# Optimization experiments

Measured on AMD Instinct MI355X. Metric: run time of the kernel, lower is better.

The kernel has to match this reference:

```python
import jax, jax.numpy as jnp
import numpy as np

D = 1024        # d_model
H = 16          # n_heads
DF = 4096       # d_ff
MAXL = 1024     # max_len
MAXSTEPS = 24   # max_steps


def setup_inputs() -> dict:
    key = jax.random.key(0)
    ks = jax.random.split(key, 10)
    B, S = 4, 1024
    s = 0.02
    f32 = jnp.float32
    return {
        "x": jax.random.normal(ks[0], (B, S, D), f32),
        "original_input": jax.random.normal(ks[1], (B, S, D), f32),
        "think_step": 5,
        "step_embed": jax.random.normal(ks[2], (MAXSTEPS, D), f32) * s,
        "Wqkv": jax.random.normal(ks[3], (D, 3 * D), f32) * s,
        "bqkv": jnp.zeros((3 * D,), f32),
        "Wout": jax.random.normal(ks[4], (D, D), f32) * s,
        "bout": jnp.zeros((D,), f32),
        "Wg": jax.random.normal(ks[5], (2 * D, D), f32) * s,
        "bg": jnp.zeros((D,), f32),
        "rel_pos_bias": jax.random.normal(ks[6], (2 * MAXL - 1,), f32) * s,
        "W1": jax.random.normal(ks[7], (D, DF), f32) * s,
        "b1": jnp.zeros((DF,), f32),
        "W2": jax.random.normal(ks[8], (DF, D), f32) * s,
        "b2": jnp.zeros((D,), f32),
        "ln1_g": jnp.ones((D,), f32),
        "ln1_b": jnp.zeros((D,), f32),
        "ln2_g": jnp.ones((D,), f32),
        "ln2_b": jnp.zeros((D,), f32),
    }


def _layer_norm(x, g, b, eps=1e-5):
    m = jnp.mean(x, axis=-1, keepdims=True)
    v = jnp.mean((x - m) ** 2, axis=-1, keepdims=True)
    return (x - m) * jax.lax.rsqrt(v + eps) * g + b


def reference(x, original_input, think_step, step_embed, Wqkv, bqkv, Wout, bout,
              Wg, bg, rel_pos_bias, W1, b1, W2, b2, ln1_g, ln1_b, ln2_g, ln2_b):
    B, S, _ = x.shape
    hd = D // H
    # gated residual input injection
    gate = jax.nn.sigmoid(jnp.concatenate([x, original_input], axis=-1) @ Wg + bg)
    x = x * (1.0 - gate) + original_input * gate
    # think-step embedding (clamped)
    step = min(int(think_step), MAXSTEPS - 1)
    x = x + step_embed[step][None, None, :]
    # qkv projection -> (3, B, H, S, hd)
    qkv = (x @ Wqkv + bqkv).reshape(B, S, 3, H, hd).transpose(2, 0, 3, 1, 4)
    q, k, v = qkv[0], qkv[1], qkv[2]
    scores = jnp.einsum('bhqd,bhkd->bhqk', q, k) * (hd ** -0.5)
    # relative position bias: dist clamped to [0, 2*MAXL-2]
    pos = jnp.arange(S)
    rel = jnp.clip(pos[:, None] - pos[None, :] + (MAXL - 1), 0, 2 * MAXL - 2)
    scores = scores + rel_pos_bias[rel][None, None]  # (B,H,S,S)
    probs = jax.nn.softmax(scores, axis=-1)
    attn = jnp.einsum('bhqk,bhkd->bhqd', probs, v)
    attn = attn.transpose(0, 2, 1, 3).reshape(B, S, D)
    attn = attn @ Wout + bout
    x = _layer_norm(x + attn, ln1_g, ln1_b)
    h = jax.nn.gelu(x @ W1 + b1, approximate=False) @ W2 + b2
    return _layer_norm(x + h, ln2_g, ln2_b)
```

## Files before the change

### kernel.cpp

```cpp
#include <hip/hip_runtime.h>
#include <hip/hip_bf16.h>
#include <math.h>

#define D_MODEL 1024
#define NH      16
#define HD      64
#define DFF     4096
#define SEQ     1024
#define BATCH   4
#define TOK     (BATCH*SEQ)
#define MAXSTEPS 24

typedef __hip_bfloat16 bf16;
typedef __attribute__((ext_vector_type(8))) short short8;
typedef __attribute__((ext_vector_type(4))) float floatx4;

__device__ __forceinline__ float b2f(bf16 v){ return __bfloat162float(v); }
__device__ __forceinline__ bf16  f2b(float v){ return __float2bfloat16(v); }

__device__ __forceinline__ void gload_lds16(const bf16* g, bf16* l){
    __builtin_amdgcn_global_load_lds((const __attribute__((address_space(1))) void*)g,
                                     (__attribute__((address_space(3))) void*)l, 16, 0, 0);
}

template<int TN, int EPI, bool SPLITK>
__global__ __launch_bounds__(256)
void mfma_gemm(const bf16* __restrict__ A, const bf16* __restrict__ Bt,
               const float* __restrict__ bias, void* __restrict__ outv,
               void* __restrict__ outv2,
               int M, int N, int K, int lda, int ldb,
               const float* __restrict__ xg, const float* __restrict__ og,
               const float* __restrict__ seg, const int* __restrict__ stepp)
{
    constexpr int NT  = TN / 32;
    constexpr int NBP = TN / 64;
    constexpr int R   = (TN == 64) ? 4 : 3;
    __shared__ bf16 As[R][128 * 32];
    __shared__ bf16 Bs[R][TN * 32];
    const int tid  = threadIdx.x;
    const int lane = tid & 63;
    const int w    = tid >> 6;
    const int wm   = w & 1, wn = w >> 1;
    const int fr   = lane & 15;
    const int q    = lane >> 4;

    if (SPLITK) {
        int z = blockIdx.z;
        A  += (size_t)z * K;
        Bt += (size_t)z * K;
    }

    const int tn_g = gridDim.x;
    const int nwg  = tn_g * gridDim.y;
    const int bid  = blockIdx.y * tn_g + blockIdx.x;
    const int o    = (bid & 7) * (nwg >> 3) + (bid >> 3);
    const int bandw = 8 * tn_g;
    const int band  = o / bandw;
    const int rr    = o - band * bandw;
    const int row0 = (band * 8 + (rr & 7)) * 128;
    const int col0 = (rr >> 3) * TN;

    const bf16* gA[2]; int sA_[2];
    #pragma unroll
    for (int p = 0; p < 2; ++p) {
        int s  = p * 256 + tid;
        int m  = s >> 2;
        int qg = (s & 3) ^ ((m >> 1) & 3);
        gA[p]  = A + (size_t)(row0 + m) * lda + qg * 8;
        sA_[p] = s * 8;
    }
    const bf16* gB[NBP]; int sB_[NBP];
    #pragma unroll
    for (int p = 0; p < NBP; ++p) {
        int s  = p * 256 + tid;
        int m  = s >> 2;
        int qg = (s & 3) ^ ((m >> 1) & 3);
        gB[p]  = Bt + (size_t)(col0 + m) * ldb + qg * 8;
        sB_[p] = s * 8;
    }

    int aoff[4], boff[NT];
    #pragma unroll
    for (int t = 0; t < 4; ++t) {
        int ml  = wm * 64 + t * 16 + fr;
        aoff[t] = (ml * 4 + (q ^ ((ml >> 1) & 3))) * 8;
    }
    #pragma unroll
    for (int t = 0; t < NT; ++t) {
        int nl  = wn * (TN / 2) + t * 16 + fr;
        boff[t] = (nl * 4 + (q ^ ((nl >> 1) & 3))) * 8;
    }

    #pragma unroll
    for (int pt = 0; pt < R - 1; ++pt) {
        #pragma unroll
        for (int p = 0; p < 2; ++p)   gload_lds16(gA[p] + pt * 32, &As[pt][sA_[p]]);
        #pragma unroll
        for (int p = 0; p < NBP; ++p) gload_lds16(gB[p] + pt * 32, &Bs[pt][sB_[p]]);
    }

    floatx4 acc[4][NT] = {};
    const int nk = K >> 5;
    int cur = 0;
    int kst = (R - 1) * 32;

    for (int t = 0; t < nk; ++t) {
        if constexpr (TN == 64) asm volatile("s_waitcnt vmcnt(6)" ::: "memory");
        else                    asm volatile("s_waitcnt vmcnt(4)" ::: "memory");
        __builtin_amdgcn_s_barrier();
        asm volatile("" ::: "memory");

        if (kst < K) {
            int sb = (cur == 0) ? (R - 1) : (cur - 1);
            #pragma unroll
            for (int p = 0; p < 2; ++p)   gload_lds16(gA[p] + kst, &As[sb][sA_[p]]);
            #pragma unroll
            for (int p = 0; p < NBP; ++p) gload_lds16(gB[p] + kst, &Bs[sb][sB_[p]]);
            kst += 32;
        }

        short8 af[4], bfg[NT];
        #pragma unroll
        for (int i = 0; i < 4; ++i)  af[i]  = *(const short8*)(&As[cur][aoff[i]]);
        #pragma unroll
        for (int j = 0; j < NT; ++j) bfg[j] = *(const short8*)(&Bs[cur][boff[j]]);
        #pragma unroll
        for (int i = 0; i < 4; ++i)
            #pragma unroll
            for (int j = 0; j < NT; ++j)
                acc[i][j] = __builtin_amdgcn_mfma_f32_16x16x32_bf16(af[i], bfg[j], acc[i][j], 0, 0, 0);

        cur = (cur == R - 1) ? 0 : (cur + 1);
    }

    void* outp = outv;
    float bscale = 1.0f;
    if (SPLITK && blockIdx.z != 0) { outp = outv2; bscale = 0.0f; }

    int st = 0;
    if (EPI == 3) {
        st = stepp[0];
        st = st < 0 ? 0 : (st > MAXSTEPS - 1 ? MAXSTEPS - 1 : st);
    }

    float bv[NT], sv[NT];
    #pragma unroll
    for (int nt = 0; nt < NT; ++nt) {
        int col = col0 + wn * (TN / 2) + nt * 16 + fr;
        bv[nt] = bias[col] * bscale;
        if (EPI == 3) sv[nt] = seg[st * D_MODEL + col];
    }
    #pragma unroll
    for (int mt = 0; mt < 4; ++mt) {
        #pragma unroll
        for (int nt = 0; nt < NT; ++nt) {
            int col = col0 + wn * (TN / 2) + nt * 16 + fr;
            #pragma unroll
            for (int r = 0; r < 4; ++r) {
                int row = row0 + wm * 64 + mt * 16 + q * 4 + r;
                float v = acc[mt][nt][r] + bv[nt];
                if (EPI == 0) {
                    ((float*)outp)[(size_t)row * N + col] = v;
                } else if (EPI == 1) {
                    ((bf16*)outp)[(size_t)row * N + col] = f2b(v);
                } else if (EPI == 2) {
                    float g = 0.5f * v * (1.0f + erff(v * 0.70710678118654752f));
                    ((bf16*)outp)[(size_t)row * N + col] = f2b(g);
                } else {
                    float g = 1.0f / (1.0f + __expf(-v));
                    size_t idx = (size_t)row * N + col;
                    float mix = xg[idx] * (1.0f - g) + og[idx] * g + sv[nt];
                    ((bf16*)outp)[idx] = f2b(mix);
                }
            }
        }
    }
}

#define NTRANS_BLOCKS 14336
__global__ __launch_bounds__(256)
void transpose_all_kernel(const float* __restrict__ Wg,   bf16* __restrict__ WgT,
                          const float* __restrict__ Wqkv, bf16* __restrict__ WqkvT,
                          const float* __restrict__ Wout, bf16* __restrict__ WoutT,
                          const float* __restrict__ W1,   bf16* __restrict__ W1T,
                          const float* __restrict__ W2,   bf16* __restrict__ W2T)
{
    __shared__ float t[32][33];
    const int bid = blockIdx.x;
    if (bid >= NTRANS_BLOCKS) return;
    const float* W; bf16* WT; int K, N, base;
    if      (bid <  2048) { W = Wg;   WT = WgT;   K = 2048; N = 1024; base = 0; }
    else if (bid <  5120) { W = Wqkv; WT = WqkvT; K = 1024; N = 3072; base = 2048; }
    else if (bid <  6144) { W = Wout; WT = WoutT; K = 1024; N = 1024; base = 5120; }
    else if (bid < 10240) { W = W1;   WT = W1T;   K = 1024; N = 4096; base = 6144; }
    else                  { W = W2;   WT = W2T;   K = 4096; N = 1024; base = 10240; }
    const int lb  = bid - base;
    const int ntx = N >> 5;
    const int n0 = (lb % ntx) * 32, k0 = (lb / ntx) * 32;
    const int tx = threadIdx.x & 31, ty = threadIdx.x >> 5;
    #pragma unroll
    for (int i = 0; i < 4; ++i)
        t[ty + i * 8][tx] = W[(size_t)(k0 + ty + i * 8) * N + n0 + tx];
    __syncthreads();
    #pragma unroll
    for (int i = 0; i < 4; ++i)
        WT[(size_t)(n0 + ty + i * 8) * K + k0 + tx] = f2b(t[tx][ty + i * 8]);
}

__global__ __launch_bounds__(256)
void vtrans_kernel(const bf16* __restrict__ qkv, bf16* __restrict__ Vt)
{
    __shared__ float t[32][33];
    const int blk = blockIdx.x;
    const int dt = blk & 1;
    const int st = (blk >> 1) & 31;
    const int h  = (blk >> 6) & 15;
    const int b  = blk >> 10;
    const int tx = threadIdx.x & 31, ty = threadIdx.x >> 5;
    #pragma unroll
    for (int i = 0; i < 4; ++i)
        t[ty + i * 8][tx] = b2f(qkv[(size_t)(b * SEQ + st * 32 + ty + i * 8) * 3072
                                    + 2048 + h * 64 + dt * 32 + tx]);
    __syncthreads();
    #pragma unroll
    for (int i = 0; i < 4; ++i)
        Vt[(size_t)((b * NH + h) * 64 + dt * 32 + ty + i * 8) * SEQ + st * 32 + tx]
            = f2b(t[tx][ty + i * 8]);
}

__global__ __launch_bounds__(256)
void xcat_kernel(const float* __restrict__ x, const float* __restrict__ orig,
                 bf16* __restrict__ xcat)
{
    int i = blockIdx.x * 256 + threadIdx.x;
    float4 xv = ((const float4*)x)[i];
    float4 ov = ((const float4*)orig)[i];
    int t = i >> 8, c4 = (i & 255) * 4;
    bf16* px = xcat + (size_t)t * 2048 + c4;
    px[0] = f2b(xv.x); px[1] = f2b(xv.y); px[2] = f2b(xv.z); px[3] = f2b(xv.w);
    bf16* po = px + 1024;
    po[0] = f2b(ov.x); po[1] = f2b(ov.y); po[2] = f2b(ov.z); po[3] = f2b(ov.w);
}

__global__ __launch_bounds__(256)
void fattn_kernel(const bf16* __restrict__ qkv, const bf16* __restrict__ Vt,
                  const float* __restrict__ relb, bf16* __restrict__ out)
{
    __shared__ bf16 KPs[128 * 64];
    __shared__ bf16 Vs [64 * 128];
    __shared__ float relb_s[1088];

    const int tid  = threadIdx.x;
    const int lane = tid & 63;
    const int w    = tid >> 6;
    const int fr   = lane & 15;
    const int quad = lane >> 4;

    const int qt = blockIdx.x & 15;
    const int h  = (blockIdx.x >> 4) & 15;
    const int b  = blockIdx.x >> 8;
    const int bq = b * SEQ;
    const int bh = b * NH + h;

    for (int i = tid; i < 1087; i += 256)
        relb_s[i] = relb[qt * 64 + i] - 8.0f;

    const int qrow = bq + qt * 64 + w * 16 + fr;
    short8 qf[2];
    {
        const bf16* qp = qkv + (size_t)qrow * 3072 + h * 64 + quad * 8;
        qf[0] = *(const short8*)(qp);
        qf[1] = *(const short8*)(qp + 32);
    }

    int ibase[4];
    #pragma unroll
    for (int r = 0; r < 4; ++r)
        ibase[r] = (w * 16 + quad * 4 + r) - fr + 1023;

    float lsum[4] = {0.f, 0.f, 0.f, 0.f};
    floatx4 accO[4];
    #pragma unroll
    for (int nt = 0; nt < 4; ++nt) accO[nt] = (floatx4){0.f, 0.f, 0.f, 0.f};

    for (int k0 = 0; k0 < SEQ; k0 += 128) {
        __syncthreads();
        #pragma unroll
        for (int it = 0; it < 4; ++it) {
            int s = it * 256 + tid;
            int key = s >> 3, cs = s & 7;
            int c = cs ^ (key & 7);
            const bf16* src = qkv + (size_t)(bq + k0 + key) * 3072 + 1024 + h * 64 + c * 8;
            gload_lds16(src, KPs + (size_t)s * 8);
        }
        #pragma unroll
        for (int it = 0; it < 4; ++it) {
            int s = it * 256 + tid;
            int row = s >> 4, cs = s & 15;
            int c = cs ^ (row & 15);
            const bf16* src = Vt + (size_t)(bh * 64 + row) * SEQ + k0 + c * 8;
            gload_lds16(src, Vs + (size_t)s * 8);
        }
        __syncthreads();

        floatx4 accS[8];
        #pragma unroll
        for (int t = 0; t < 8; ++t) accS[t] = (floatx4){0.f, 0.f, 0.f, 0.f};
        __builtin_amdgcn_s_setprio(1);
        #pragma unroll
        for (int t = 0; t < 8; ++t) {
            int row = t * 16 + fr;
            #pragma unroll
            for (int ks = 0; ks < 2; ++ks) {
                int slot = (ks * 4 + quad) ^ (row & 7);
                short8 kf = *(const short8*)(KPs + (size_t)row * 64 + slot * 8);
                accS[t] = __builtin_amdgcn_mfma_f32_16x16x32_bf16(qf[ks], kf, accS[t], 0, 0, 0);
            }
        }
        __builtin_amdgcn_s_setprio(0);

        __syncthreads();

        bf16* Ps = KPs + w * 2048;
        #pragma unroll
        for (int t = 0; t < 8; ++t) {
            int keyl = t * 16 + fr;
            int cbase = keyl >> 3, koff = keyl & 7;
            #pragma unroll
            for (int r = 0; r < 4; ++r) {
                float bias = relb_s[ibase[r] - k0 - t * 16];
                float p = __expf(fmaf(accS[t][r], 0.125f, bias));
                lsum[r] += p;
                int row = quad * 4 + r;
                int slot = cbase ^ (row & 15);
                Ps[(size_t)row * 128 + slot * 8 + koff] = f2b(p);
            }
        }

        __builtin_amdgcn_s_setprio(1);
        #pragma unroll
        for (int ks = 0; ks < 4; ++ks) {
            int slotp = (ks * 4 + quad) ^ (fr & 15);
            short8 pf = *(const short8*)(Ps + (size_t)fr * 128 + slotp * 8);
            #pragma unroll
            for (int nt = 0; nt < 4; ++nt) {
                int vrow = nt * 16 + fr;
                int slotv = (ks * 4 + quad) ^ (vrow & 15);
                short8 vf = *(const short8*)(Vs + (size_t)vrow * 128 + slotv * 8);
                accO[nt] = __builtin_amdgcn_mfma_f32_16x16x32_bf16(pf, vf, accO[nt], 0, 0, 0);
            }
        }
        __builtin_amdgcn_s_setprio(0);
    }

    float inv[4];
    #pragma unroll
    for (int r = 0; r < 4; ++r) {
        float v = lsum[r];
        v += __shfl_xor(v, 1); v += __shfl_xor(v, 2);
        v += __shfl_xor(v, 4); v += __shfl_xor(v, 8);
        inv[r] = 1.0f / v;
    }

    #pragma unroll
    for (int nt = 0; nt < 4; ++nt) {
        int col = h * 64 + nt * 16 + fr;
        #pragma unroll
        for (int r = 0; r < 4; ++r) {
            int t = bq + qt * 64 + w * 16 + quad * 4 + r;
            out[(size_t)t * D_MODEL + col] = f2b(accO[nt][r] * inv[r]);
        }
    }
}

template<bool OUT_BF16, bool HAS2>
__global__ __launch_bounds__(256)
void ln_kernel(const bf16* __restrict__ a, const float* __restrict__ add,
               const float* __restrict__ add2,
               const float* __restrict__ g, const float* __restrict__ bb,
               void* __restrict__ outv)
{
    __shared__ float red[256];
    __shared__ float red2[256];
    const int row = blockIdx.x;
    const int tid = threadIdx.x;
    float s[4];
    float lsum = 0.f, lsq = 0.f;
    #pragma unroll
    for (int u = 0; u < 4; ++u) {
        int i = tid + 256 * u;
        float v = b2f(a[row * D_MODEL + i]) + add[row * D_MODEL + i];
        if (HAS2) v += add2[row * D_MODEL + i];
        s[u] = v; lsum += v; lsq += v * v;
    }
    red[tid] = lsum; red2[tid] = lsq; __syncthreads();
    for (int s2 = 128; s2 > 0; s2 >>= 1) {
        if (tid < s2) { red[tid] += red[tid + s2]; red2[tid] += red2[tid + s2]; }
        __syncthreads();
    }
    float mean = red[0] * (1.0f / D_MODEL);
    float var  = red2[0] * (1.0f / D_MODEL) - mean * mean;
    float rs = rsqrtf(var + 1e-5f);
    #pragma unroll
    for (int u = 0; u < 4; ++u) {
        int i = tid + 256 * u;
        float o = (s[u] - mean) * rs * g[i] + bb[i];
        if (OUT_BF16) ((bf16*)outv)[row * D_MODEL + i] = f2b(o);
        else          ((float*)outv)[row * D_MODEL + i] = o;
    }
}

extern "C" void kernel_launch(void* const* d_in, const int* in_sizes, int n_in,
                              void* d_out, int out_size, void* d_ws, size_t ws_size,
                              hipStream_t stream)
{
    const float* x     = (const float*)d_in[0];
    const float* orig  = (const float*)d_in[1];
    const int*   step  = (const int*)  d_in[2];
    const float* se    = (const float*)d_in[3];
    const float* Wqkv  = (const float*)d_in[4];
    const float* bqkv  = (const float*)d_in[5];
    const float* Wout  = (const float*)d_in[6];
    const float* bout  = (const float*)d_in[7];
    const float* Wg    = (const float*)d_in[8];
    const float* bg    = (const float*)d_in[9];
    const float* relb  = (const float*)d_in[10];
    const float* W1    = (const float*)d_in[11];
    const float* b1    = (const float*)d_in[12];
    const float* W2    = (const float*)d_in[13];
    const float* b2    = (const float*)d_in[14];
    const float* ln1g  = (const float*)d_in[15];
    const float* ln1b  = (const float*)d_in[16];
    const float* ln2g  = (const float*)d_in[17];
    const float* ln2b  = (const float*)d_in[18];

    char* ws = (char*)d_ws;
    bf16* WgT   = (bf16*)(ws);
    bf16* WqkvT = (bf16*)(ws + ( 4u << 20));
    bf16* WoutT = (bf16*)(ws + (10u << 20));
    bf16* W1T   = (bf16*)(ws + (12u << 20));
    bf16* W2T   = (bf16*)(ws + (20u << 20));
    bf16* xw    = (bf16*)(ws + (28u << 20));
    bf16* xcat  = (bf16*)(ws + (36u << 20));
    bf16* attnb = (bf16*)(ws + (36u << 20));
    bf16* h     = (bf16*)(ws + (44u << 20));
    bf16* qkvb  = (bf16*)(ws + (52u << 20));
    float* tmp2 = (float*)(ws);
    bf16* Vt    = (bf16*)d_out;
    float* tmp  = (float*)d_out;

    dim3 blk(256);

    transpose_all_kernel<<<NTRANS_BLOCKS, blk, 0, stream>>>(Wg, WgT, Wqkv, WqkvT,
                                                    Wout, WoutT, W1, W1T, W2, W2T);
    xcat_kernel<<<TOK, blk, 0, stream>>>(x, orig, xcat);

    mfma_gemm<64, 3, false><<<dim3(D_MODEL/64, TOK/128), blk, 0, stream>>>(
        xcat, WgT, bg, xw, nullptr, TOK, D_MODEL, 2*D_MODEL, 2*D_MODEL, 2*D_MODEL,
        x, orig, se, step);

    mfma_gemm<128, 1, false><<<dim3(3*D_MODEL/128, TOK/128), blk, 0, stream>>>(
        xw, WqkvT, bqkv, qkvb, nullptr, TOK, 3*D_MODEL, D_MODEL, D_MODEL, D_MODEL,
        nullptr, nullptr, nullptr, nullptr);

    vtrans_kernel<<<BATCH*NH*64, blk, 0, stream>>>(qkvb, Vt);

    fattn_kernel<<<BATCH*NH*(SEQ/64), blk, 0, stream>>>(qkvb, Vt, relb, attnb);

    mfma_gemm<64, 0, false><<<dim3(D_MODEL/64, TOK/128), blk, 0, stream>>>(
        attnb, WoutT, bout, tmp, nullptr, TOK, D_MODEL, D_MODEL, D_MODEL, D_MODEL,
        nullptr, nullptr, nullptr, nullptr);

    ln_kernel<true, false><<<TOK, blk, 0, stream>>>(xw, tmp, nullptr, ln1g, ln1b, xw);

    mfma_gemm<128, 2, false><<<dim3(DFF/128, TOK/128), blk, 0, stream>>>(
        xw, W1T, b1, h, nullptr, TOK, DFF, D_MODEL, D_MODEL, D_MODEL,
        nullptr, nullptr, nullptr, nullptr);

    mfma_gemm<128, 0, true><<<dim3(D_MODEL/128, TOK/128, 2), blk, 0, stream>>>(
        h, W2T, b2, tmp, tmp2, TOK, D_MODEL, DFF/2, DFF, DFF,
        nullptr, nullptr, nullptr, nullptr);

    ln_kernel<false, true><<<TOK, blk, 0, stream>>>(xw, tmp, tmp2, ln2g, ln2b, d_out);
}
```

Before: 430.2 us.

## Fuse V transpose into QKV GEMM epilogue and add wide-tile GELU GEMM

Adds a new epilogue mode to the QKV GEMM that writes the V columns directly in transposed per-head layout, which removes the separate V-transpose kernel and its extra pass over global memory. The FFN up-projection moves to a dedicated 256x128-tile GEMM with a triple-buffered LDS pipeline, swizzled LDS layout, tile remapping for L2 locality and a fused GELU epilogue. The transposed V stores are strided and poorly coalesced. The larger tile uses more registers and LDS, which can limit occupancy.

```diff
diff --git a/kernel.cpp b/kernel.cpp
--- a/kernel.cpp
+++ b/kernel.cpp
@@ -166,12 +166,138 @@
                 } else if (EPI == 2) {
                     float g = 0.5f * v * (1.0f + erff(v * 0.70710678118654752f));
                     ((bf16*)outp)[(size_t)row * N + col] = f2b(g);
-                } else {
+                } else if (EPI == 3) {
                     float g = 1.0f / (1.0f + __expf(-v));
                     size_t idx = (size_t)row * N + col;
                     float mix = xg[idx] * (1.0f - g) + og[idx] * g + sv[nt];
                     ((bf16*)outp)[idx] = f2b(mix);
+                } else {
+                    if (col0 < 2048) {
+                        ((bf16*)outp)[(size_t)row * N + col] = f2b(v);
+                    } else {
+                        int b = row >> 10, s = row & 1023;
+                        int hh = (col - 2048) >> 6, d = (col - 2048) & 63;
+                        ((bf16*)outv2)[((size_t)((b * NH + hh) * 64 + d)) * SEQ + s] = f2b(v);
+                    }
                 }
+            }
+        }
+    }
+}
+
+__global__ __launch_bounds__(256, 2)
+void gemm_wide_gelu(const bf16* __restrict__ A, const bf16* __restrict__ Bt,
+                    const float* __restrict__ bias, bf16* __restrict__ out,
+                    int M, int N, int K)
+{
+    constexpr int R = 3;
+    __shared__ bf16 As[R][256 * 32];
+    __shared__ bf16 Bs[R][128 * 32];
+    const int tid  = threadIdx.x;
+    const int lane = tid & 63;
+    const int w    = tid >> 6;
+    const int wm   = w & 1, wn = w >> 1;
+    const int fr   = lane & 15;
+    const int q    = lane >> 4;
+
+    const int tn_g = gridDim.x;
+    const int nwg  = tn_g * gridDim.y;
+    const int bid  = blockIdx.y * tn_g + blockIdx.x;
+    const int o    = (bid & 7) * (nwg >> 3) + (bid >> 3);
+    const int bandw = 8 * tn_g;
+    const int band  = o / bandw;
+    const int rr    = o - band * bandw;
+    const int row0 = (band * 8 + (rr & 7)) * 256;
+    const int col0 = (rr >> 3) * 128;
+
+    const bf16* gA[4]; int sA_[4];
+    #pragma unroll
+    for (int p = 0; p < 4; ++p) {
+        int s  = p * 256 + tid;
+        int m  = s >> 2;
+        int qg = (s & 3) ^ ((m >> 1) & 3);
+        gA[p]  = A + (size_t)(row0 + m) * K + qg * 8;
+        sA_[p] = s * 8;
+    }
+    const bf16* gB[2]; int sB_[2];
+    #pragma unroll
+    for (int p = 0; p < 2; ++p) {
+        int s  = p * 256 + tid;
+        int m  = s >> 2;
+        int qg = (s & 3) ^ ((m >> 1) & 3);
+        gB[p]  = Bt + (size_t)(col0 + m) * K + qg * 8;
+        sB_[p] = s * 8;
+    }
+
+    int aoff[8], boff[4];
+    #pragma unroll
+    for (int t = 0; t < 8; ++t) {
+        int ml  = wm * 128 + t * 16 + fr;
+        aoff[t] = (ml * 4 + (q ^ ((ml >> 1) & 3))) * 8;
+    }
+    #pragma unroll
+    for (int t = 0; t < 4; ++t) {
+        int nl  = wn * 64 + t * 16 + fr;
+        boff[t] = (nl * 4 + (q ^ ((nl >> 1) & 3))) * 8;
+    }
+
+    #pragma unroll
+    for (int pt = 0; pt < R - 1; ++pt) {
+        #pragma unroll
+        for (int p = 0; p < 4; ++p) gload_lds16(gA[p] + pt * 32, &As[pt][sA_[p]]);
+        #pragma unroll
+        for (int p = 0; p < 2; ++p) gload_lds16(gB[p] + pt * 32, &Bs[pt][sB_[p]]);
+    }
+
+    floatx4 acc[8][4] = {};
+    const int nk = K >> 5;
+    int cur = 0;
+    int kst = (R - 1) * 32;
+
+    for (int t = 0; t < nk; ++t) {
+        asm volatile("s_waitcnt vmcnt(6)" ::: "memory");
+        __builtin_amdgcn_s_barrier();
+        asm volatile("" ::: "memory");
+
+        if (kst < K) {
+            int sb = (cur == 0) ? (R - 1) : (cur - 1);
+            #pragma unroll
+            for (int p = 0; p < 4; ++p) gload_lds16(gA[p] + kst, &As[sb][sA_[p]]);
+            #pragma unroll
+            for (int p = 0; p < 2; ++p) gload_lds16(gB[p] + kst, &Bs[sb][sB_[p]]);
+            kst += 32;
+        }
+
+        short8 af[8], bfg[4];
+        #pragma unroll
+        for (int i = 0; i < 8; ++i) af[i]  = *(const short8*)(&As[cur][aoff[i]]);
+        #pragma unroll
+        for (int j = 0; j < 4; ++j) bfg[j] = *(const short8*)(&Bs[cur][boff[j]]);
+        __builtin_amdgcn_s_setprio(1);
+        #pragma unroll
+        for (int i = 0; i < 8; ++i)
+            #pragma unroll
+            for (int j = 0; j < 4; ++j)
+                acc[i][j] = __builtin_amdgcn_mfma_f32_16x16x32_bf16(af[i], bfg[j], acc[i][j], 0, 0, 0);
+        __builtin_amdgcn_s_setprio(0);
+
+        cur = (cur == R - 1) ? 0 : (cur + 1);
+    }
+
+    float bv[4];
+    #pragma unroll
+    for (int j = 0; j < 4; ++j) bv[j] = bias[col0 + wn * 64 + j * 16 + fr];
+    #pragma unroll
+    for (int mt = 0; mt < 8; ++mt) {
+        #pragma unroll
+        for (int nt = 0; nt < 4; ++nt) {
+            int col = col0 + wn * 64 + nt * 16 + fr;
+            #pragma unroll
+            for (int r = 0; r < 4; ++r) {
+                int row = row0 + wm * 128 + mt * 16 + q * 4 + r;
+                float v = acc[mt][nt][r] + bv[nt];
+                float g = 0.5f * v * (1.0f + erff(v * 0.70710678118654752f));
+                out[(size_t)row * N + col] = f2b(g);
             }
         }
     }
@@ -205,27 +331,6 @@
     #pragma unroll
     for (int i = 0; i < 4; ++i)
         WT[(size_t)(n0 + ty + i * 8) * K + k0 + tx] = f2b(t[tx][ty + i * 8]);
-}
-
-__global__ __launch_bounds__(256)
-void vtrans_kernel(const bf16* __restrict__ qkv, bf16* __restrict__ Vt)
-{
-    __shared__ float t[32][33];
-    const int blk = blockIdx.x;
-    const int dt = blk & 1;
-    const int st = (blk >> 1) & 31;
-    const int h  = (blk >> 6) & 15;
-    const int b  = blk >> 10;
-    const int tx = threadIdx.x & 31, ty = threadIdx.x >> 5;
-    #pragma unroll
-    for (int i = 0; i < 4; ++i)
-        t[ty + i * 8][tx] = b2f(qkv[(size_t)(b * SEQ + st * 32 + ty + i * 8) * 3072
-                                    + 2048 + h * 64 + dt * 32 + tx]);
-    __syncthreads();
-    #pragma unroll
-    for (int i = 0; i < 4; ++i)
-        Vt[(size_t)((b * NH + h) * 64 + dt * 32 + ty + i * 8) * SEQ + st * 32 + tx]
-            = f2b(t[tx][ty + i * 8]);
 }
 
 __global__ __launch_bounds__(256)
@@ -459,11 +564,9 @@
         xcat, WgT, bg, xw, nullptr, TOK, D_MODEL, 2*D_MODEL, 2*D_MODEL, 2*D_MODEL,
         x, orig, se, step);
 
-    mfma_gemm<128, 1, false><<<dim3(3*D_MODEL/128, TOK/128), blk, 0, stream>>>(
-        xw, WqkvT, bqkv, qkvb, nullptr, TOK, 3*D_MODEL, D_MODEL, D_MODEL, D_MODEL,
+    mfma_gemm<128, 4, false><<<dim3(3*D_MODEL/128, TOK/128), blk, 0, stream>>>(
+        xw, WqkvT, bqkv, qkvb, Vt, TOK, 3*D_MODEL, D_MODEL, D_MODEL, D_MODEL,
         nullptr, nullptr, nullptr, nullptr);
-
-    vtrans_kernel<<<BATCH*NH*64, blk, 0, stream>>>(qkvb, Vt);
 
     fattn_kernel<<<BATCH*NH*(SEQ/64), blk, 0, stream>>>(qkvb, Vt, relb, attnb);
 
@@ -473,9 +576,8 @@
 
     ln_kernel<true, false><<<TOK, blk, 0, stream>>>(xw, tmp, nullptr, ln1g, ln1b, xw);
 
-    mfma_gemm<128, 2, false><<<dim3(DFF/128, TOK/128), blk, 0, stream>>>(
-        xw, W1T, b1, h, nullptr, TOK, DFF, D_MODEL, D_MODEL, D_MODEL,
-        nullptr, nullptr, nullptr, nullptr);
+    gemm_wide_gelu<<<dim3(DFF/128, TOK/256), blk, 0, stream>>>(
+        xw, W1T, b1, h, TOK, DFF, D_MODEL);
 
     mfma_gemm<128, 0, true><<<dim3(D_MODEL/128, TOK/128, 2), blk, 0, stream>>>(
         h, W2T, b2, tmp, tmp2, TOK, D_MODEL, DFF/2, DFF, DFF,
```

Result: no change. 429.5 us (-0.2%).
